# Kernel tuning notes

Measured on AMD Instinct MI355X. Metric: run time of the kernel, lower is better.

The kernel has to match this reference:

```python
import jax, jax.numpy as jnp
import numpy as np

N_NODES = 100000
N_EDGES = 1600000
C_IN = 32
C_OUT = 32


def setup_inputs() -> dict:
    key = jax.random.key(0)
    k1, k2, k3 = jax.random.split(key, 3)
    x = jax.random.normal(k1, (N_NODES, C_IN), dtype=jnp.float32)
    edge_index = jax.random.randint(k2, (2, N_EDGES), 0, N_NODES, dtype=jnp.int32)
    # Glorot-like init for the GCN linear weight [Cout, Cin]
    W = jax.random.normal(k3, (C_OUT, C_IN), dtype=jnp.float32) * (1.0 / np.sqrt(C_IN))
    b = jnp.zeros((C_OUT,), dtype=jnp.float32)
    return {"x": x, "edge_index": edge_index, "W": W, "b": b}


def reference(x, edge_index, W, b):
    # PyG GCNConv: add self-loops, symmetric normalization, linear, scatter-add, bias.
    n = x.shape[0]
    loops = jnp.arange(n, dtype=edge_index.dtype)
    row = jnp.concatenate([edge_index[0], loops])  # source nodes
    col = jnp.concatenate([edge_index[1], loops])  # target nodes

    # degree over targets (with self loops), deg^{-1/2} with inf -> 0
    ones = jnp.ones(row.shape[0], dtype=x.dtype)
    deg = jax.ops.segment_sum(ones, col, num_segments=n)
    dinv = jnp.where(deg > 0, jax.lax.rsqrt(jnp.maximum(deg, 1e-12)), 0.0)
    norm = dinv[row] * dinv[col]  # [E + N]

    h = x @ W.T  # [N, Cout] linear transform before propagation
    msg = h[row] * norm[:, None]  # gather + scale, [E+N, Cout]
    out = jax.ops.segment_sum(msg, col, num_segments=n)  # scatter-add to targets
    return out + b
```

## Files before the change

### kernel.cpp

```cpp
#include <hip/hip_runtime.h>

#define NN 100000
#define NE 1600000
#define C 32

#define SHIFT 8
#define BINW 256
#define NBIN ((NN + BINW - 1) / BINW)
#define EPB 8192
#define NCHK ((NE + EPB - 1) / EPB)
#define SLACK 56
#define QPC 14
#define CAPT (NCHK * SLACK)
#define SCAP 5120

__device__ __forceinline__ unsigned bf16rne(float f) {
    unsigned u = __float_as_uint(f);
    return (u + 0x7fffu + ((u >> 16) & 1u)) >> 16;
}
__device__ __forceinline__ float blo(unsigned u) { return __uint_as_float(u << 16); }
__device__ __forceinline__ float bhi(unsigned u) { return __uint_as_float(u & 0xffff0000u); }


__global__ __launch_bounds__(1024) void k_bin(const int* __restrict__ ei,
                                              int* __restrict__ tmp,
                                              int* __restrict__ cfill) {
    __shared__ int lcur[NBIN];
    int b = blockIdx.x, t = threadIdx.x;
    if (t < NBIN) lcur[t] = t * CAPT + b * SLACK;
    __syncthreads();
    int e0 = b * EPB, e1 = min(e0 + EPB, NE);
    const int4* src4 = (const int4*)ei;
    const int4* col4 = (const int4*)(ei + NE);
    for (int q = (e0 >> 2) + t; q < (e1 >> 2); q += 1024) {
        int4 s = src4[q];
        int4 c = col4[q];
        int p0 = atomicAdd(&lcur[c.x >> SHIFT], 1);
        tmp[p0] = (s.x << SHIFT) | (c.x & (BINW - 1));
        int p1 = atomicAdd(&lcur[c.y >> SHIFT], 1);
        tmp[p1] = (s.y << SHIFT) | (c.y & (BINW - 1));
        int p2 = atomicAdd(&lcur[c.z >> SHIFT], 1);
        tmp[p2] = (s.z << SHIFT) | (c.z & (BINW - 1));
        int p3 = atomicAdd(&lcur[c.w >> SHIFT], 1);
        tmp[p3] = (s.w << SHIFT) | (c.w & (BINW - 1));
    }
    __syncthreads();
    if (t < NBIN)
        cfill[b * NBIN + t] = lcur[t] - (t * CAPT + b * SLACK);
}

__global__ __launch_bounds__(1024) void k_degLin(const int* __restrict__ cfill,
                                                 const int* __restrict__ tmp,
                                                 const float* __restrict__ x,
                                                 const float* __restrict__ W,
                                                 int* __restrict__ deg,
                                                 unsigned* __restrict__ hu) {
    __shared__ int ccnt[NCHK];
    __shared__ int cnt[BINW];
    __shared__ float Ws[C][C + 1];
    __shared__ float xs[BINW][C];
    int bin = blockIdx.x, t = threadIdx.x;
    if (t < NCHK) ccnt[t] = cfill[t * NBIN + bin];
    if (t < BINW) cnt[t] = 0;
    Ws[t >> 5][t & 31] = W[t];
    for (int i = t; i < BINW * C; i += 1024) {
        int idx = (bin << SHIFT) * C + i;
        xs[i >> 5][i & 31] = (idx < NN * C) ? x[idx] : 0.0f;
    }
    __syncthreads();
    const int4* tp4 = (const int4*)tmp + bin * (CAPT >> 2);
    for (int q = t; q < (CAPT >> 2); q += 1024) {
        int chunk = q / QPC;
        int off = (q - chunk * QPC) << 2;
        int fill = ccnt[chunk];
        if (off < fill) {
            int4 v = tp4[q];
            atomicAdd(&cnt[v.x & (BINW - 1)], 1);
            if (off + 1 < fill) atomicAdd(&cnt[v.y & (BINW - 1)], 1);
            if (off + 2 < fill) atomicAdd(&cnt[v.z & (BINW - 1)], 1);
            if (off + 3 < fill) atomicAdd(&cnt[v.w & (BINW - 1)], 1);
        }
    }
    __syncthreads();
    if (t < BINW) {
        int node = (bin << SHIFT) + t;
        if (node < NN) deg[node] = cnt[t];
    }
    int m = t & 15, nl0 = t >> 4;
#pragma unroll
    for (int rep = 0; rep < 4; ++rep) {
        int nl = nl0 + (rep << 6);
        int node = (bin << SHIFT) + nl;
        if (node < NN) {
            float a0 = 0.0f, a1 = 0.0f;
#pragma unroll
            for (int k = 0; k < C; ++k) {
                float xv = xs[nl][k];
                a0 += xv * Ws[2 * m][k];
                a1 += xv * Ws[2 * m + 1][k];
            }
            float d = rsqrtf(1.0f + (float)cnt[nl]);
            hu[node * 16 + m] = bf16rne(a0 * d) | (bf16rne(a1 * d) << 16);
        }
    }
}

#define AGG_T 1024
__global__ __launch_bounds__(AGG_T) void k_placeAgg(const int* __restrict__ cfill,
                                                    const int* __restrict__ tmp,
                                                    const int* __restrict__ deg,
                                                    const uint4* __restrict__ hu4,
                                                    const float* __restrict__ b,
                                                    float* __restrict__ out) {
    __shared__ int ccnt[NCHK];
    __shared__ int dg[BINW];
    __shared__ int lbase[BINW];
    __shared__ int lcur[BINW];
    __shared__ int lsort[SCAP];
    __shared__ int wtot[4], wbase[4];
    int bin = blockIdx.x, t = threadIdx.x;
    if (t < NCHK) ccnt[t] = cfill[t * NBIN + bin];
    if (t < BINW) {
        int node = (bin << SHIFT) + t;
        dg[t] = (node < NN) ? deg[node] : 0;
    }
    __syncthreads();
    int lane = t & 63, w4 = t >> 6;
    int cv = 0, v = 0;
    if (t < BINW) {
        cv = dg[t];
        v = cv;
#pragma unroll
        for (int d = 1; d < 64; d <<= 1) {
            int u = __shfl_up(v, d);
            if (lane >= d) v += u;
        }
        if (lane == 63) wtot[w4] = v;
    }
    __syncthreads();
    if (t == 0) {
        int r = 0;
#pragma unroll
        for (int k = 0; k < 4; ++k) { wbase[k] = r; r += wtot[k]; }
    }
    __syncthreads();
    if (t < BINW) {
        int loc = wbase[w4] + v - cv;
        lbase[t] = loc;
        lcur[t] = loc;
    }
    __syncthreads();
    const int4* tp4 = (const int4*)tmp + bin * (CAPT >> 2);
    for (int q = t; q < (CAPT >> 2); q += AGG_T) {
        int chunk = q / QPC;
        int off = (q - chunk * QPC) << 2;
        int fill = ccnt[chunk];
        if (off < fill) {
            int4 e = tp4[q];
            lsort[atomicAdd(&lcur[e.x & (BINW - 1)], 1)] = e.x >> SHIFT;
            if (off + 1 < fill) lsort[atomicAdd(&lcur[e.y & (BINW - 1)], 1)] = e.y >> SHIFT;
            if (off + 2 < fill) lsort[atomicAdd(&lcur[e.z & (BINW - 1)], 1)] = e.z >> SHIFT;
            if (off + 3 < fill) lsort[atomicAdd(&lcur[e.w & (BINW - 1)], 1)] = e.w >> SHIFT;
        }
    }
    __syncthreads();
    int g = t >> 2, m = t & 3;
    int beg = lbase[g], cnt = dg[g];
    float s0 = 0.0f, s1 = 0.0f, s2 = 0.0f, s3 = 0.0f;
    float s4 = 0.0f, s5 = 0.0f, s6 = 0.0f, s7 = 0.0f;
    int j = beg, jend = beg + cnt;
    for (; j + 3 < jend; j += 4) {
        int r0 = lsort[j], r1 = lsort[j + 1], r2 = lsort[j + 2], r3 = lsort[j + 3];
        uint4 u0 = hu4[r0 * 4 + m];
        uint4 u1 = hu4[r1 * 4 + m];
        uint4 u2 = hu4[r2 * 4 + m];
        uint4 u3 = hu4[r3 * 4 + m];
        s0 += blo(u0.x); s1 += bhi(u0.x); s2 += blo(u0.y); s3 += bhi(u0.y);
        s4 += blo(u0.z); s5 += bhi(u0.z); s6 += blo(u0.w); s7 += bhi(u0.w);
        s0 += blo(u1.x); s1 += bhi(u1.x); s2 += blo(u1.y); s3 += bhi(u1.y);
        s4 += blo(u1.z); s5 += bhi(u1.z); s6 += blo(u1.w); s7 += bhi(u1.w);
        s0 += blo(u2.x); s1 += bhi(u2.x); s2 += blo(u2.y); s3 += bhi(u2.y);
        s4 += blo(u2.z); s5 += bhi(u2.z); s6 += blo(u2.w); s7 += bhi(u2.w);
        s0 += blo(u3.x); s1 += bhi(u3.x); s2 += blo(u3.y); s3 += bhi(u3.y);
        s4 += blo(u3.z); s5 += bhi(u3.z); s6 += blo(u3.w); s7 += bhi(u3.w);
    }
    for (; j < jend; ++j) {
        uint4 u = hu4[lsort[j] * 4 + m];
        s0 += blo(u.x); s1 += bhi(u.x); s2 += blo(u.y); s3 += bhi(u.y);
        s4 += blo(u.z); s5 += bhi(u.z); s6 += blo(u.w); s7 += bhi(u.w);
    }
    int node = (bin << SHIFT) + g;
    if (node < NN) {
        float dn = rsqrtf(1.0f + (float)cnt);
        uint4 us = hu4[node * 4 + m];
        float4 b0 = ((const float4*)b)[2 * m];
        float4 b1 = ((const float4*)b)[2 * m + 1];
        float4 o0, o1;
        o0.x = b0.x + dn * (s0 + blo(us.x));
        o0.y = b0.y + dn * (s1 + bhi(us.x));
        o0.z = b0.z + dn * (s2 + blo(us.y));
        o0.w = b0.w + dn * (s3 + bhi(us.y));
        o1.x = b1.x + dn * (s4 + blo(us.z));
        o1.y = b1.y + dn * (s5 + bhi(us.z));
        o1.z = b1.z + dn * (s6 + blo(us.w));
        o1.w = b1.w + dn * (s7 + bhi(us.w));
        ((float4*)out)[node * 8 + 2 * m] = o0;
        ((float4*)out)[node * 8 + 2 * m + 1] = o1;
    }
}


extern "C" void kernel_launch(void* const* d_in, const int* in_sizes, int n_in,
                              void* d_out, int out_size, void* d_ws, size_t ws_size,
                              hipStream_t stream) {
    const float* x  = (const float*)d_in[0];
    const int*   ei = (const int*)d_in[1];
    const float* W  = (const float*)d_in[2];
    const float* b  = (const float*)d_in[3];
    float* out = (float*)d_out;

    char* ws = (char*)d_ws;
    size_t o = 0;
    int*      tmp   = (int*)(ws + o);      o += (size_t)NBIN * CAPT * 4;   o = (o + 255) & ~(size_t)255;
    unsigned* hu    = (unsigned*)(ws + o); o += (size_t)NN * 16 * 4;       o = (o + 255) & ~(size_t)255;
    int*      cfill = (int*)(ws + o);      o += (size_t)NCHK * NBIN * 4;   o = (o + 255) & ~(size_t)255;
    int*      deg   = (int*)(ws + o);

    k_bin<<<NCHK, 1024, 0, stream>>>(ei, tmp, cfill);
    k_degLin<<<NBIN, 1024, 0, stream>>>(cfill, tmp, x, W, deg, hu);
    k_placeAgg<<<NBIN, AGG_T, 0, stream>>>(cfill, tmp, deg, (const uint4*)hu, b, out);
}
```

Before: 121.4 us.

## Fuse binning, degree/linear and aggregation into one cooperative kernel

Replaces three launches with a single cooperative kernel that uses grid.sync() between binning, the degree/linear stage and aggregation. Degree counts stay in shared memory rather than being written to and reread from a global deg buffer. The chunk size is halved and the slack shrunk so the chunk count matches the bin count, letting one grid serve every phase with 512-thread blocks. The aim is to cut inter-kernel launch gaps and redundant global traffic, at the price of grid-wide barriers and a requirement that all blocks be co-resident.

```diff
diff --git a/kernel.cpp b/kernel.cpp
--- a/kernel.cpp
+++ b/kernel.cpp
@@ -1,4 +1,7 @@
 #include <hip/hip_runtime.h>
+#include <hip/hip_cooperative_groups.h>
+
+namespace cg = cooperative_groups;
 
 #define NN 100000
 #define NE 1600000
@@ -7,10 +10,10 @@
 #define SHIFT 8
 #define BINW 256
 #define NBIN ((NN + BINW - 1) / BINW)
-#define EPB 8192
+#define EPB 4096
 #define NCHK ((NE + EPB - 1) / EPB)
-#define SLACK 56
-#define QPC 14
+#define SLACK 36
+#define QPC (SLACK / 4)
 #define CAPT (NCHK * SLACK)
 #define SCAP 5120
 
@@ -21,55 +24,62 @@
 __device__ __forceinline__ float blo(unsigned u) { return __uint_as_float(u << 16); }
 __device__ __forceinline__ float bhi(unsigned u) { return __uint_as_float(u & 0xffff0000u); }
 
-
-__global__ __launch_bounds__(1024) void k_bin(const int* __restrict__ ei,
-                                              int* __restrict__ tmp,
-                                              int* __restrict__ cfill) {
-    __shared__ int lcur[NBIN];
-    int b = blockIdx.x, t = threadIdx.x;
-    if (t < NBIN) lcur[t] = t * CAPT + b * SLACK;
-    __syncthreads();
-    int e0 = b * EPB, e1 = min(e0 + EPB, NE);
-    const int4* src4 = (const int4*)ei;
-    const int4* col4 = (const int4*)(ei + NE);
-    for (int q = (e0 >> 2) + t; q < (e1 >> 2); q += 1024) {
-        int4 s = src4[q];
-        int4 c = col4[q];
-        int p0 = atomicAdd(&lcur[c.x >> SHIFT], 1);
-        tmp[p0] = (s.x << SHIFT) | (c.x & (BINW - 1));
-        int p1 = atomicAdd(&lcur[c.y >> SHIFT], 1);
-        tmp[p1] = (s.y << SHIFT) | (c.y & (BINW - 1));
-        int p2 = atomicAdd(&lcur[c.z >> SHIFT], 1);
-        tmp[p2] = (s.z << SHIFT) | (c.z & (BINW - 1));
-        int p3 = atomicAdd(&lcur[c.w >> SHIFT], 1);
-        tmp[p3] = (s.w << SHIFT) | (c.w & (BINW - 1));
-    }
-    __syncthreads();
-    if (t < NBIN)
-        cfill[b * NBIN + t] = lcur[t] - (t * CAPT + b * SLACK);
-}
-
-__global__ __launch_bounds__(1024) void k_degLin(const int* __restrict__ cfill,
-                                                 const int* __restrict__ tmp,
+__global__ __launch_bounds__(512, 4) void k_mega(const int* __restrict__ ei,
                                                  const float* __restrict__ x,
                                                  const float* __restrict__ W,
-                                                 int* __restrict__ deg,
-                                                 unsigned* __restrict__ hu) {
-    __shared__ int ccnt[NCHK];
+                                                 const float* __restrict__ bias,
+                                                 int* __restrict__ tmp,
+                                                 int* __restrict__ cfill,
+                                                 unsigned* __restrict__ hu,
+                                                 float* __restrict__ out) {
+    __shared__ int ccnt[NBIN];
     __shared__ int cnt[BINW];
+    __shared__ int lbase[BINW];
+    __shared__ int lcur[BINW];
+    __shared__ int wtot[4], wbase[4];
     __shared__ float Ws[C][C + 1];
     __shared__ float xs[BINW][C];
-    int bin = blockIdx.x, t = threadIdx.x;
-    if (t < NCHK) ccnt[t] = cfill[t * NBIN + bin];
+    __shared__ int lsort[SCAP];
+    cg::grid_group grid = cg::this_grid();
+    int blk = blockIdx.x, t = threadIdx.x;
+
+    if (t < NBIN) ccnt[t] = t * CAPT + blk * SLACK;
+    __syncthreads();
+    {
+        int e0 = blk * EPB, e1 = min(e0 + EPB, NE);
+        const int4* src4 = (const int4*)ei;
+        const int4* col4 = (const int4*)(ei + NE);
+        for (int q = (e0 >> 2) + t; q < (e1 >> 2); q += 512) {
+            int4 s = src4[q];
+            int4 c = col4[q];
+            int p0 = atomicAdd(&ccnt[c.x >> SHIFT], 1);
+            tmp[p0] = (s.x << SHIFT) | (c.x & (BINW - 1));
+            int p1 = atomicAdd(&ccnt[c.y >> SHIFT], 1);
+            tmp[p1] = (s.y << SHIFT) | (c.y & (BINW - 1));
+            int p2 = atomicAdd(&ccnt[c.z >> SHIFT], 1);
+            tmp[p2] = (s.z << SHIFT) | (c.z & (BINW - 1));
+            int p3 = atomicAdd(&ccnt[c.w >> SHIFT], 1);
+            tmp[p3] = (s.w << SHIFT) | (c.w & (BINW - 1));
+        }
+    }
+    __syncthreads();
+    if (t < NBIN)
+        cfill[blk * NBIN + t] = ccnt[t] - (t * CAPT + blk * SLACK);
+
+    grid.sync();
+
+    int bin = blk;
+    if (t < NBIN) ccnt[t] = cfill[t * NBIN + bin];
     if (t < BINW) cnt[t] = 0;
     Ws[t >> 5][t & 31] = W[t];
-    for (int i = t; i < BINW * C; i += 1024) {
+    Ws[(t + 512) >> 5][t & 31] = W[t + 512];
+    for (int i = t; i < BINW * C; i += 512) {
         int idx = (bin << SHIFT) * C + i;
         xs[i >> 5][i & 31] = (idx < NN * C) ? x[idx] : 0.0f;
     }
     __syncthreads();
     const int4* tp4 = (const int4*)tmp + bin * (CAPT >> 2);
-    for (int q = t; q < (CAPT >> 2); q += 1024) {
+    for (int q = t; q < (CAPT >> 2); q += 512) {
         int chunk = q / QPC;
         int off = (q - chunk * QPC) << 2;
         int fill = ccnt[chunk];
@@ -82,53 +92,10 @@
         }
     }
     __syncthreads();
-    if (t < BINW) {
-        int node = (bin << SHIFT) + t;
-        if (node < NN) deg[node] = cnt[t];
-    }
-    int m = t & 15, nl0 = t >> 4;
-#pragma unroll
-    for (int rep = 0; rep < 4; ++rep) {
-        int nl = nl0 + (rep << 6);
-        int node = (bin << SHIFT) + nl;
-        if (node < NN) {
-            float a0 = 0.0f, a1 = 0.0f;
-#pragma unroll
-            for (int k = 0; k < C; ++k) {
-                float xv = xs[nl][k];
-                a0 += xv * Ws[2 * m][k];
-                a1 += xv * Ws[2 * m + 1][k];
-            }
-            float d = rsqrtf(1.0f + (float)cnt[nl]);
-            hu[node * 16 + m] = bf16rne(a0 * d) | (bf16rne(a1 * d) << 16);
-        }
-    }
-}
-
-#define AGG_T 1024
-__global__ __launch_bounds__(AGG_T) void k_placeAgg(const int* __restrict__ cfill,
-                                                    const int* __restrict__ tmp,
-                                                    const int* __restrict__ deg,
-                                                    const uint4* __restrict__ hu4,
-                                                    const float* __restrict__ b,
-                                                    float* __restrict__ out) {
-    __shared__ int ccnt[NCHK];
-    __shared__ int dg[BINW];
-    __shared__ int lbase[BINW];
-    __shared__ int lcur[BINW];
-    __shared__ int lsort[SCAP];
-    __shared__ int wtot[4], wbase[4];
-    int bin = blockIdx.x, t = threadIdx.x;
-    if (t < NCHK) ccnt[t] = cfill[t * NBIN + bin];
-    if (t < BINW) {
-        int node = (bin << SHIFT) + t;
-        dg[t] = (node < NN) ? deg[node] : 0;
-    }
-    __syncthreads();
     int lane = t & 63, w4 = t >> 6;
     int cv = 0, v = 0;
     if (t < BINW) {
-        cv = dg[t];
+        cv = cnt[t];
         v = cv;
 #pragma unroll
         for (int d = 1; d < 64; d <<= 1) {
@@ -150,8 +117,7 @@
         lcur[t] = loc;
     }
     __syncthreads();
-    const int4* tp4 = (const int4*)tmp + bin * (CAPT >> 2);
-    for (int q = t; q < (CAPT >> 2); q += AGG_T) {
+    for (int q = t; q < (CAPT >> 2); q += 512) {
         int chunk = q / QPC;
         int off = (q - chunk * QPC) << 2;
         int fill = ccnt[chunk];
@@ -163,49 +129,75 @@
             if (off + 3 < fill) lsort[atomicAdd(&lcur[e.w & (BINW - 1)], 1)] = e.w >> SHIFT;
         }
     }
-    __syncthreads();
+    {
+        int m = t & 15, nl0 = t >> 4;
+#pragma unroll
+        for (int rep = 0; rep < 8; ++rep) {
+            int nl = nl0 + (rep << 5);
+            int node = (bin << SHIFT) + nl;
+            if (node < NN) {
+                float a0 = 0.0f, a1 = 0.0f;
+#pragma unroll
+                for (int k = 0; k < C; ++k) {
+                    float xv = xs[nl][k];
+                    a0 += xv * Ws[2 * m][k];
+                    a1 += xv * Ws[2 * m + 1][k];
+                }
+                float d = rsqrtf(1.0f + (float)cnt[nl]);
+                hu[node * 16 + m] = bf16rne(a0 * d) | (bf16rne(a1 * d) << 16);
+            }
+        }
+    }
+
+    grid.sync();
+
+    const uint4* hu4 = (const uint4*)hu;
     int g = t >> 2, m = t & 3;
-    int beg = lbase[g], cnt = dg[g];
-    float s0 = 0.0f, s1 = 0.0f, s2 = 0.0f, s3 = 0.0f;
-    float s4 = 0.0f, s5 = 0.0f, s6 = 0.0f, s7 = 0.0f;
-    int j = beg, jend = beg + cnt;
-    for (; j + 3 < jend; j += 4) {
-        int r0 = lsort[j], r1 = lsort[j + 1], r2 = lsort[j + 2], r3 = lsort[j + 3];
-        uint4 u0 = hu4[r0 * 4 + m];
-        uint4 u1 = hu4[r1 * 4 + m];
-        uint4 u2 = hu4[r2 * 4 + m];
-        uint4 u3 = hu4[r3 * 4 + m];
-        s0 += blo(u0.x); s1 += bhi(u0.x); s2 += blo(u0.y); s3 += bhi(u0.y);
-        s4 += blo(u0.z); s5 += bhi(u0.z); s6 += blo(u0.w); s7 += bhi(u0.w);
-        s0 += blo(u1.x); s1 += bhi(u1.x); s2 += blo(u1.y); s3 += bhi(u1.y);
-        s4 += blo(u1.z); s5 += bhi(u1.z); s6 += blo(u1.w); s7 += bhi(u1.w);
-        s0 += blo(u2.x); s1 += bhi(u2.x); s2 += blo(u2.y); s3 += bhi(u2.y);
-        s4 += blo(u2.z); s5 += bhi(u2.z); s6 += blo(u2.w); s7 += bhi(u2.w);
-        s0 += blo(u3.x); s1 += bhi(u3.x); s2 += blo(u3.y); s3 += bhi(u3.y);
-        s4 += blo(u3.z); s5 += bhi(u3.z); s6 += blo(u3.w); s7 += bhi(u3.w);
-    }
-    for (; j < jend; ++j) {
-        uint4 u = hu4[lsort[j] * 4 + m];
-        s0 += blo(u.x); s1 += bhi(u.x); s2 += blo(u.y); s3 += bhi(u.y);
-        s4 += blo(u.z); s5 += bhi(u.z); s6 += blo(u.w); s7 += bhi(u.w);
-    }
-    int node = (bin << SHIFT) + g;
-    if (node < NN) {
-        float dn = rsqrtf(1.0f + (float)cnt);
-        uint4 us = hu4[node * 4 + m];
-        float4 b0 = ((const float4*)b)[2 * m];
-        float4 b1 = ((const float4*)b)[2 * m + 1];
-        float4 o0, o1;
-        o0.x = b0.x + dn * (s0 + blo(us.x));
-        o0.y = b0.y + dn * (s1 + bhi(us.x));
-        o0.z = b0.z + dn * (s2 + blo(us.y));
-        o0.w = b0.w + dn * (s3 + bhi(us.y));
-        o1.x = b1.x + dn * (s4 + blo(us.z));
-        o1.y = b1.y + dn * (s5 + bhi(us.z));
-        o1.z = b1.z + dn * (s6 + blo(us.w));
-        o1.w = b1.w + dn * (s7 + bhi(us.w));
-        ((float4*)out)[node * 8 + 2 * m] = o0;
-        ((float4*)out)[node * 8 + 2 * m + 1] = o1;
+#pragma unroll
+    for (int rr = 0; rr < 2; ++rr) {
+        int loc = g + rr * 128;
+        int node = (bin << SHIFT) + loc;
+        int beg = lbase[loc], cdeg = cnt[loc];
+        float s0 = 0.0f, s1 = 0.0f, s2 = 0.0f, s3 = 0.0f;
+        float s4 = 0.0f, s5 = 0.0f, s6 = 0.0f, s7 = 0.0f;
+        int j = beg, jend = beg + cdeg;
+        for (; j + 3 < jend; j += 4) {
+            int r0 = lsort[j], r1 = lsort[j + 1], r2 = lsort[j + 2], r3 = lsort[j + 3];
+            uint4 u0 = hu4[r0 * 4 + m];
+            uint4 u1 = hu4[r1 * 4 + m];
+            uint4 u2 = hu4[r2 * 4 + m];
+            uint4 u3 = hu4[r3 * 4 + m];
+            s0 += blo(u0.x); s1 += bhi(u0.x); s2 += blo(u0.y); s3 += bhi(u0.y);
+            s4 += blo(u0.z); s5 += bhi(u0.z); s6 += blo(u0.w); s7 += bhi(u0.w);
+            s0 += blo(u1.x); s1 += bhi(u1.x); s2 += blo(u1.y); s3 += bhi(u1.y);
+            s4 += blo(u1.z); s5 += bhi(u1.z); s6 += blo(u1.w); s7 += bhi(u1.w);
+            s0 += blo(u2.x); s1 += bhi(u2.x); s2 += blo(u2.y); s3 += bhi(u2.y);
+            s4 += blo(u2.z); s5 += bhi(u2.z); s6 += blo(u2.w); s7 += bhi(u2.w);
+            s0 += blo(u3.x); s1 += bhi(u3.x); s2 += blo(u3.y); s3 += bhi(u3.y);
+            s4 += blo(u3.z); s5 += bhi(u3.z); s6 += blo(u3.w); s7 += bhi(u3.w);
+        }
+        for (; j < jend; ++j) {
+            uint4 u = hu4[lsort[j] * 4 + m];
+            s0 += blo(u.x); s1 += bhi(u.x); s2 += blo(u.y); s3 += bhi(u.y);
+            s4 += blo(u.z); s5 += bhi(u.z); s6 += blo(u.w); s7 += bhi(u.w);
+        }
+        if (node < NN) {
+            float dn = rsqrtf(1.0f + (float)cdeg);
+            uint4 us = hu4[node * 4 + m];
+            float4 b0 = ((const float4*)bias)[2 * m];
+            float4 b1 = ((const float4*)bias)[2 * m + 1];
+            float4 o0, o1;
+            o0.x = b0.x + dn * (s0 + blo(us.x));
+            o0.y = b0.y + dn * (s1 + bhi(us.x));
+            o0.z = b0.z + dn * (s2 + blo(us.y));
+            o0.w = b0.w + dn * (s3 + bhi(us.y));
+            o1.x = b1.x + dn * (s4 + blo(us.z));
+            o1.y = b1.y + dn * (s5 + bhi(us.z));
+            o1.z = b1.z + dn * (s6 + blo(us.w));
+            o1.w = b1.w + dn * (s7 + bhi(us.w));
+            ((float4*)out)[node * 8 + 2 * m] = o0;
+            ((float4*)out)[node * 8 + 2 * m + 1] = o1;
+        }
     }
 }
 
@@ -223,10 +215,10 @@
     size_t o = 0;
     int*      tmp   = (int*)(ws + o);      o += (size_t)NBIN * CAPT * 4;   o = (o + 255) & ~(size_t)255;
     unsigned* hu    = (unsigned*)(ws + o); o += (size_t)NN * 16 * 4;       o = (o + 255) & ~(size_t)255;
-    int*      cfill = (int*)(ws + o);      o += (size_t)NCHK * NBIN * 4;   o = (o + 255) & ~(size_t)255;
-    int*      deg   = (int*)(ws + o);
-
-    k_bin<<<NCHK, 1024, 0, stream>>>(ei, tmp, cfill);
-    k_degLin<<<NBIN, 1024, 0, stream>>>(cfill, tmp, x, W, deg, hu);
-    k_placeAgg<<<NBIN, AGG_T, 0, stream>>>(cfill, tmp, deg, (const uint4*)hu, b, out);
+    int*      cfill = (int*)(ws + o);
+
+    void* args[] = { (void*)&ei, (void*)&x, (void*)&W, (void*)&b,
+                     (void*)&tmp, (void*)&cfill, (void*)&hu, (void*)&out };
+    hipLaunchCooperativeKernel((const void*)k_mega, dim3(NBIN), dim3(512),
+                               args, 0, stream);
 }
```

New measurement: 241.0 us. 1.99x slower.

## Move per-bin counting sort into degree/linear kernel, aggregate with small blocks

Applied to the files above, without the earlier changes.

Performs the per-bin prefix scan and placement of source indices inside the degree/linear kernel, writing a sorted CSR-like index array to global memory with packed offset and count per node. The aggregation kernel becomes a lightweight 256-thread kernel reading those offsets and indices from global memory. This removes the second pass over the binned edge buffer and the large shared-memory sort from the aggregation kernel, allowing higher occupancy there. In exchange it adds a global write and read of the sorted index array, and ties tail latency of the first kernel to the extra placement pass.

```diff
diff --git a/kernel.cpp b/kernel.cpp
--- a/kernel.cpp
+++ b/kernel.cpp
@@ -49,14 +49,17 @@
         cfill[b * NBIN + t] = lcur[t] - (t * CAPT + b * SLACK);
 }
 
-__global__ __launch_bounds__(1024) void k_degLin(const int* __restrict__ cfill,
-                                                 const int* __restrict__ tmp,
-                                                 const float* __restrict__ x,
-                                                 const float* __restrict__ W,
-                                                 int* __restrict__ deg,
-                                                 unsigned* __restrict__ hu) {
+__global__ __launch_bounds__(1024) void k_degLinPlace(const int* __restrict__ cfill,
+                                                      const int* __restrict__ tmp,
+                                                      const float* __restrict__ x,
+                                                      const float* __restrict__ W,
+                                                      int* __restrict__ srt,
+                                                      int* __restrict__ off,
+                                                      unsigned* __restrict__ hu) {
     __shared__ int ccnt[NCHK];
     __shared__ int cnt[BINW];
+    __shared__ int lcur[BINW];
+    __shared__ int wtot[4], wbase[4];
     __shared__ float Ws[C][C + 1];
     __shared__ float xs[BINW][C];
     int bin = blockIdx.x, t = threadIdx.x;
@@ -71,20 +74,55 @@
     const int4* tp4 = (const int4*)tmp + bin * (CAPT >> 2);
     for (int q = t; q < (CAPT >> 2); q += 1024) {
         int chunk = q / QPC;
-        int off = (q - chunk * QPC) << 2;
+        int o = (q - chunk * QPC) << 2;
         int fill = ccnt[chunk];
-        if (off < fill) {
+        if (o < fill) {
             int4 v = tp4[q];
             atomicAdd(&cnt[v.x & (BINW - 1)], 1);
-            if (off + 1 < fill) atomicAdd(&cnt[v.y & (BINW - 1)], 1);
-            if (off + 2 < fill) atomicAdd(&cnt[v.z & (BINW - 1)], 1);
-            if (off + 3 < fill) atomicAdd(&cnt[v.w & (BINW - 1)], 1);
-        }
-    }
-    __syncthreads();
+            if (o + 1 < fill) atomicAdd(&cnt[v.y & (BINW - 1)], 1);
+            if (o + 2 < fill) atomicAdd(&cnt[v.z & (BINW - 1)], 1);
+            if (o + 3 < fill) atomicAdd(&cnt[v.w & (BINW - 1)], 1);
+        }
+    }
+    __syncthreads();
+    int lane = t & 63, w4 = t >> 6;
+    int cv = 0, v = 0;
     if (t < BINW) {
+        cv = cnt[t];
+        v = cv;
+#pragma unroll
+        for (int d = 1; d < 64; d <<= 1) {
+            int u = __shfl_up(v, d);
+            if (lane >= d) v += u;
+        }
+        if (lane == 63) wtot[w4] = v;
+    }
+    __syncthreads();
+    if (t == 0) {
+        int r = 0;
+#pragma unroll
+        for (int k = 0; k < 4; ++k) { wbase[k] = r; r += wtot[k]; }
+    }
+    __syncthreads();
+    if (t < BINW) {
+        int loc = wbase[w4] + v - cv;
+        lcur[t] = loc;
         int node = (bin << SHIFT) + t;
-        if (node < NN) deg[node] = cnt[t];
+        if (node < NN) off[node] = loc | (cv << 16);
+    }
+    __syncthreads();
+    int sbase = bin * SCAP;
+    for (int q = t; q < (CAPT >> 2); q += 1024) {
+        int chunk = q / QPC;
+        int o = (q - chunk * QPC) << 2;
+        int fill = ccnt[chunk];
+        if (o < fill) {
+            int4 e = tp4[q];
+            srt[sbase + atomicAdd(&lcur[e.x & (BINW - 1)], 1)] = e.x >> SHIFT;
+            if (o + 1 < fill) srt[sbase + atomicAdd(&lcur[e.y & (BINW - 1)], 1)] = e.y >> SHIFT;
+            if (o + 2 < fill) srt[sbase + atomicAdd(&lcur[e.z & (BINW - 1)], 1)] = e.z >> SHIFT;
+            if (o + 3 < fill) srt[sbase + atomicAdd(&lcur[e.w & (BINW - 1)], 1)] = e.w >> SHIFT;
+        }
     }
     int m = t & 15, nl0 = t >> 4;
 #pragma unroll
@@ -105,72 +143,23 @@
     }
 }
 
-#define AGG_T 1024
-__global__ __launch_bounds__(AGG_T) void k_placeAgg(const int* __restrict__ cfill,
-                                                    const int* __restrict__ tmp,
-                                                    const int* __restrict__ deg,
-                                                    const uint4* __restrict__ hu4,
-                                                    const float* __restrict__ b,
-                                                    float* __restrict__ out) {
-    __shared__ int ccnt[NCHK];
-    __shared__ int dg[BINW];
-    __shared__ int lbase[BINW];
-    __shared__ int lcur[BINW];
-    __shared__ int lsort[SCAP];
-    __shared__ int wtot[4], wbase[4];
-    int bin = blockIdx.x, t = threadIdx.x;
-    if (t < NCHK) ccnt[t] = cfill[t * NBIN + bin];
-    if (t < BINW) {
-        int node = (bin << SHIFT) + t;
-        dg[t] = (node < NN) ? deg[node] : 0;
-    }
-    __syncthreads();
-    int lane = t & 63, w4 = t >> 6;
-    int cv = 0, v = 0;
-    if (t < BINW) {
-        cv = dg[t];
-        v = cv;
-#pragma unroll
-        for (int d = 1; d < 64; d <<= 1) {
-            int u = __shfl_up(v, d);
-            if (lane >= d) v += u;
-        }
-        if (lane == 63) wtot[w4] = v;
-    }
-    __syncthreads();
-    if (t == 0) {
-        int r = 0;
-#pragma unroll
-        for (int k = 0; k < 4; ++k) { wbase[k] = r; r += wtot[k]; }
-    }
-    __syncthreads();
-    if (t < BINW) {
-        int loc = wbase[w4] + v - cv;
-        lbase[t] = loc;
-        lcur[t] = loc;
-    }
-    __syncthreads();
-    const int4* tp4 = (const int4*)tmp + bin * (CAPT >> 2);
-    for (int q = t; q < (CAPT >> 2); q += AGG_T) {
-        int chunk = q / QPC;
-        int off = (q - chunk * QPC) << 2;
-        int fill = ccnt[chunk];
-        if (off < fill) {
-            int4 e = tp4[q];
-            lsort[atomicAdd(&lcur[e.x & (BINW - 1)], 1)] = e.x >> SHIFT;
-            if (off + 1 < fill) lsort[atomicAdd(&lcur[e.y & (BINW - 1)], 1)] = e.y >> SHIFT;
-            if (off + 2 < fill) lsort[atomicAdd(&lcur[e.z & (BINW - 1)], 1)] = e.z >> SHIFT;
-            if (off + 3 < fill) lsort[atomicAdd(&lcur[e.w & (BINW - 1)], 1)] = e.w >> SHIFT;
-        }
-    }
-    __syncthreads();
+__global__ __launch_bounds__(256) void k_agg(const int* __restrict__ off,
+                                             const int* __restrict__ srt,
+                                             const uint4* __restrict__ hu4,
+                                             const float* __restrict__ b,
+                                             float* __restrict__ out) {
+    int t = threadIdx.x;
     int g = t >> 2, m = t & 3;
-    int beg = lbase[g], cnt = dg[g];
+    int node = blockIdx.x * 64 + g;
+    if (node >= NN) return;
+    int ov = off[node];
+    int beg = (node >> SHIFT) * SCAP + (ov & 0xffff);
+    int cnt = ov >> 16;
     float s0 = 0.0f, s1 = 0.0f, s2 = 0.0f, s3 = 0.0f;
     float s4 = 0.0f, s5 = 0.0f, s6 = 0.0f, s7 = 0.0f;
     int j = beg, jend = beg + cnt;
     for (; j + 3 < jend; j += 4) {
-        int r0 = lsort[j], r1 = lsort[j + 1], r2 = lsort[j + 2], r3 = lsort[j + 3];
+        int r0 = srt[j], r1 = srt[j + 1], r2 = srt[j + 2], r3 = srt[j + 3];
         uint4 u0 = hu4[r0 * 4 + m];
         uint4 u1 = hu4[r1 * 4 + m];
         uint4 u2 = hu4[r2 * 4 + m];
@@ -185,28 +174,25 @@
         s4 += blo(u3.z); s5 += bhi(u3.z); s6 += blo(u3.w); s7 += bhi(u3.w);
     }
     for (; j < jend; ++j) {
-        uint4 u = hu4[lsort[j] * 4 + m];
+        uint4 u = hu4[srt[j] * 4 + m];
         s0 += blo(u.x); s1 += bhi(u.x); s2 += blo(u.y); s3 += bhi(u.y);
         s4 += blo(u.z); s5 += bhi(u.z); s6 += blo(u.w); s7 += bhi(u.w);
     }
-    int node = (bin << SHIFT) + g;
-    if (node < NN) {
-        float dn = rsqrtf(1.0f + (float)cnt);
-        uint4 us = hu4[node * 4 + m];
-        float4 b0 = ((const float4*)b)[2 * m];
-        float4 b1 = ((const float4*)b)[2 * m + 1];
-        float4 o0, o1;
-        o0.x = b0.x + dn * (s0 + blo(us.x));
-        o0.y = b0.y + dn * (s1 + bhi(us.x));
-        o0.z = b0.z + dn * (s2 + blo(us.y));
-        o0.w = b0.w + dn * (s3 + bhi(us.y));
-        o1.x = b1.x + dn * (s4 + blo(us.z));
-        o1.y = b1.y + dn * (s5 + bhi(us.z));
-        o1.z = b1.z + dn * (s6 + blo(us.w));
-        o1.w = b1.w + dn * (s7 + bhi(us.w));
-        ((float4*)out)[node * 8 + 2 * m] = o0;
-        ((float4*)out)[node * 8 + 2 * m + 1] = o1;
-    }
+    float dn = rsqrtf(1.0f + (float)cnt);
+    uint4 us = hu4[node * 4 + m];
+    float4 b0 = ((const float4*)b)[2 * m];
+    float4 b1 = ((const float4*)b)[2 * m + 1];
+    float4 o0, o1;
+    o0.x = b0.x + dn * (s0 + blo(us.x));
+    o0.y = b0.y + dn * (s1 + bhi(us.x));
+    o0.z = b0.z + dn * (s2 + blo(us.y));
+    o0.w = b0.w + dn * (s3 + bhi(us.y));
+    o1.x = b1.x + dn * (s4 + blo(us.z));
+    o1.y = b1.y + dn * (s5 + bhi(us.z));
+    o1.z = b1.z + dn * (s6 + blo(us.w));
+    o1.w = b1.w + dn * (s7 + bhi(us.w));
+    ((float4*)out)[node * 8 + 2 * m] = o0;
+    ((float4*)out)[node * 8 + 2 * m + 1] = o1;
 }
 
 
@@ -222,11 +208,12 @@
     char* ws = (char*)d_ws;
     size_t o = 0;
     int*      tmp   = (int*)(ws + o);      o += (size_t)NBIN * CAPT * 4;   o = (o + 255) & ~(size_t)255;
+    int*      srt   = (int*)(ws + o);      o += (size_t)NBIN * SCAP * 4;   o = (o + 255) & ~(size_t)255;
     unsigned* hu    = (unsigned*)(ws + o); o += (size_t)NN * 16 * 4;       o = (o + 255) & ~(size_t)255;
     int*      cfill = (int*)(ws + o);      o += (size_t)NCHK * NBIN * 4;   o = (o + 255) & ~(size_t)255;
-    int*      deg   = (int*)(ws + o);
+    int*      off   = (int*)(ws + o);
 
     k_bin<<<NCHK, 1024, 0, stream>>>(ei, tmp, cfill);
-    k_degLin<<<NBIN, 1024, 0, stream>>>(cfill, tmp, x, W, deg, hu);
-    k_placeAgg<<<NBIN, AGG_T, 0, stream>>>(cfill, tmp, deg, (const uint4*)hu, b, out);
-}
+    k_degLinPlace<<<NBIN, 1024, 0, stream>>>(cfill, tmp, x, W, srt, off, hu);
+    k_agg<<<(NN + 63) / 64, 256, 0, stream>>>(off, srt, (const uint4*)hu, b, out);
+}
```

Result: slower. 129.0 us (+6.3%).

## Overlap linear transform with edge binning in one kernel, scale by degree later

Applied to the files above, without the earlier changes.

Moves the x@W^T linear transform out of the degree kernel into extra blocks of the binning kernel, so the GEMM runs concurrently with edge binning instead of after it. The degree kernel then only counts degrees and rescales the stored bf16 h in place by deg^-1/2. This adds an extra read-modify-write pass over h and a second bf16 rounding (unscaled, then scaled), which slightly changes numerics. The binning grid also becomes larger and mixes two kinds of block.

```diff
diff --git a/kernel.cpp b/kernel.cpp
--- a/kernel.cpp
+++ b/kernel.cpp
@@ -13,6 +13,7 @@
 #define QPC 14
 #define CAPT (NCHK * SLACK)
 #define SCAP 5120
+#define NLIN ((NN + 63) / 64)
 
 __device__ __forceinline__ unsigned bf16rne(float f) {
     unsigned u = __float_as_uint(f);
@@ -22,75 +23,47 @@
 __device__ __forceinline__ float bhi(unsigned u) { return __uint_as_float(u & 0xffff0000u); }
 
 
-__global__ __launch_bounds__(1024) void k_bin(const int* __restrict__ ei,
-                                              int* __restrict__ tmp,
-                                              int* __restrict__ cfill) {
-    __shared__ int lcur[NBIN];
-    int b = blockIdx.x, t = threadIdx.x;
-    if (t < NBIN) lcur[t] = t * CAPT + b * SLACK;
-    __syncthreads();
-    int e0 = b * EPB, e1 = min(e0 + EPB, NE);
-    const int4* src4 = (const int4*)ei;
-    const int4* col4 = (const int4*)(ei + NE);
-    for (int q = (e0 >> 2) + t; q < (e1 >> 2); q += 1024) {
-        int4 s = src4[q];
-        int4 c = col4[q];
-        int p0 = atomicAdd(&lcur[c.x >> SHIFT], 1);
-        tmp[p0] = (s.x << SHIFT) | (c.x & (BINW - 1));
-        int p1 = atomicAdd(&lcur[c.y >> SHIFT], 1);
-        tmp[p1] = (s.y << SHIFT) | (c.y & (BINW - 1));
-        int p2 = atomicAdd(&lcur[c.z >> SHIFT], 1);
-        tmp[p2] = (s.z << SHIFT) | (c.z & (BINW - 1));
-        int p3 = atomicAdd(&lcur[c.w >> SHIFT], 1);
-        tmp[p3] = (s.w << SHIFT) | (c.w & (BINW - 1));
-    }
-    __syncthreads();
-    if (t < NBIN)
-        cfill[b * NBIN + t] = lcur[t] - (t * CAPT + b * SLACK);
-}
-
-__global__ __launch_bounds__(1024) void k_degLin(const int* __restrict__ cfill,
-                                                 const int* __restrict__ tmp,
+__global__ __launch_bounds__(1024) void k_binLin(const int* __restrict__ ei,
                                                  const float* __restrict__ x,
                                                  const float* __restrict__ W,
-                                                 int* __restrict__ deg,
+                                                 int* __restrict__ tmp,
+                                                 int* __restrict__ cfill,
                                                  unsigned* __restrict__ hu) {
-    __shared__ int ccnt[NCHK];
-    __shared__ int cnt[BINW];
+    __shared__ int lcur[NBIN];
     __shared__ float Ws[C][C + 1];
-    __shared__ float xs[BINW][C];
-    int bin = blockIdx.x, t = threadIdx.x;
-    if (t < NCHK) ccnt[t] = cfill[t * NBIN + bin];
-    if (t < BINW) cnt[t] = 0;
-    Ws[t >> 5][t & 31] = W[t];
-    for (int i = t; i < BINW * C; i += 1024) {
-        int idx = (bin << SHIFT) * C + i;
-        xs[i >> 5][i & 31] = (idx < NN * C) ? x[idx] : 0.0f;
-    }
-    __syncthreads();
-    const int4* tp4 = (const int4*)tmp + bin * (CAPT >> 2);
-    for (int q = t; q < (CAPT >> 2); q += 1024) {
-        int chunk = q / QPC;
-        int off = (q - chunk * QPC) << 2;
-        int fill = ccnt[chunk];
-        if (off < fill) {
-            int4 v = tp4[q];
-            atomicAdd(&cnt[v.x & (BINW - 1)], 1);
-            if (off + 1 < fill) atomicAdd(&cnt[v.y & (BINW - 1)], 1);
-            if (off + 2 < fill) atomicAdd(&cnt[v.z & (BINW - 1)], 1);
-            if (off + 3 < fill) atomicAdd(&cnt[v.w & (BINW - 1)], 1);
-        }
-    }
-    __syncthreads();
-    if (t < BINW) {
-        int node = (bin << SHIFT) + t;
-        if (node < NN) deg[node] = cnt[t];
-    }
-    int m = t & 15, nl0 = t >> 4;
-#pragma unroll
-    for (int rep = 0; rep < 4; ++rep) {
-        int nl = nl0 + (rep << 6);
-        int node = (bin << SHIFT) + nl;
+    __shared__ float xs[64][C];
+    int b = blockIdx.x, t = threadIdx.x;
+    if (b < NCHK) {
+        if (t < NBIN) lcur[t] = t * CAPT + b * SLACK;
+        __syncthreads();
+        int e0 = b * EPB, e1 = min(e0 + EPB, NE);
+        const int4* src4 = (const int4*)ei;
+        const int4* col4 = (const int4*)(ei + NE);
+        for (int q = (e0 >> 2) + t; q < (e1 >> 2); q += 1024) {
+            int4 s = src4[q];
+            int4 c = col4[q];
+            int p0 = atomicAdd(&lcur[c.x >> SHIFT], 1);
+            tmp[p0] = (s.x << SHIFT) | (c.x & (BINW - 1));
+            int p1 = atomicAdd(&lcur[c.y >> SHIFT], 1);
+            tmp[p1] = (s.y << SHIFT) | (c.y & (BINW - 1));
+            int p2 = atomicAdd(&lcur[c.z >> SHIFT], 1);
+            tmp[p2] = (s.z << SHIFT) | (c.z & (BINW - 1));
+            int p3 = atomicAdd(&lcur[c.w >> SHIFT], 1);
+            tmp[p3] = (s.w << SHIFT) | (c.w & (BINW - 1));
+        }
+        __syncthreads();
+        if (t < NBIN)
+            cfill[b * NBIN + t] = lcur[t] - (t * CAPT + b * SLACK);
+    } else {
+        int node0 = (b - NCHK) * 64;
+        Ws[t >> 5][t & 31] = W[t];
+        for (int i = t; i < 64 * C; i += 1024) {
+            int idx = node0 * C + i;
+            xs[i >> 5][i & 31] = (idx < NN * C) ? x[idx] : 0.0f;
+        }
+        __syncthreads();
+        int m = t & 15, nl = t >> 4;
+        int node = node0 + nl;
         if (node < NN) {
             float a0 = 0.0f, a1 = 0.0f;
 #pragma unroll
@@ -99,9 +72,49 @@
                 a0 += xv * Ws[2 * m][k];
                 a1 += xv * Ws[2 * m + 1][k];
             }
-            float d = rsqrtf(1.0f + (float)cnt[nl]);
-            hu[node * 16 + m] = bf16rne(a0 * d) | (bf16rne(a1 * d) << 16);
-        }
+            hu[node * 16 + m] = bf16rne(a0) | (bf16rne(a1) << 16);
+        }
+    }
+}
+
+__global__ __launch_bounds__(1024) void k_degScale(const int* __restrict__ cfill,
+                                                   const int* __restrict__ tmp,
+                                                   int* __restrict__ deg,
+                                                   unsigned* __restrict__ hu) {
+    __shared__ int ccnt[NCHK];
+    __shared__ int cnt[BINW];
+    __shared__ float di[BINW];
+    int bin = blockIdx.x, t = threadIdx.x;
+    if (t < NCHK) ccnt[t] = cfill[t * NBIN + bin];
+    if (t < BINW) cnt[t] = 0;
+    __syncthreads();
+    const int4* tp4 = (const int4*)tmp + bin * (CAPT >> 2);
+    for (int q = t; q < (CAPT >> 2); q += 1024) {
+        int chunk = q / QPC;
+        int o = (q - chunk * QPC) << 2;
+        int fill = ccnt[chunk];
+        if (o < fill) {
+            int4 v = tp4[q];
+            atomicAdd(&cnt[v.x & (BINW - 1)], 1);
+            if (o + 1 < fill) atomicAdd(&cnt[v.y & (BINW - 1)], 1);
+            if (o + 2 < fill) atomicAdd(&cnt[v.z & (BINW - 1)], 1);
+            if (o + 3 < fill) atomicAdd(&cnt[v.w & (BINW - 1)], 1);
+        }
+    }
+    __syncthreads();
+    if (t < BINW) {
+        int cv = cnt[t];
+        di[t] = rsqrtf(1.0f + (float)cv);
+        int node = (bin << SHIFT) + t;
+        if (node < NN) deg[node] = cv;
+    }
+    __syncthreads();
+    unsigned* hb = hu + (size_t)(bin << SHIFT) * 16;
+    int lim = (min(NN - (bin << SHIFT), BINW)) * 16;
+    for (int i = t; i < lim; i += 1024) {
+        unsigned u = hb[i];
+        float d = di[i >> 4];
+        hb[i] = bf16rne(blo(u) * d) | (bf16rne(bhi(u) * d) << 16);
     }
 }
 
@@ -226,7 +239,7 @@
     int*      cfill = (int*)(ws + o);      o += (size_t)NCHK * NBIN * 4;   o = (o + 255) & ~(size_t)255;
     int*      deg   = (int*)(ws + o);
 
-    k_bin<<<NCHK, 1024, 0, stream>>>(ei, tmp, cfill);
-    k_degLin<<<NBIN, 1024, 0, stream>>>(cfill, tmp, x, W, deg, hu);
+    k_binLin<<<NCHK + NLIN, 1024, 0, stream>>>(ei, x, W, tmp, cfill, hu);
+    k_degScale<<<NBIN, 1024, 0, stream>>>(cfill, tmp, deg, hu);
     k_placeAgg<<<NBIN, AGG_T, 0, stream>>>(cfill, tmp, deg, (const uint4*)hu, b, out);
 }
```

Result: no change. 119.9 us (-1.2%).
